# Kernel tuning notes

Hardware: AMD Instinct MI355X
Metric: run time of the kernel (lower is better)

## Reference

```python
import jax, jax.numpy as jnp
import numpy as np

E = 8192   # line-graph nodes (edges of g)
N = 4096   # graph nodes
FIN = 64   # in_feats
FOUT = 64  # out_feats
H = FOUT // 2
BN_EPS = 1e-5


def _linear_params(k, fan_in):
    kw, kb = jax.random.split(k)
    s = 1.0 / np.sqrt(fan_in)
    w = jax.random.uniform(kw, (H, fan_in), jnp.float32, -s, s)
    b = jax.random.uniform(kb, (H,), jnp.float32, -s, s)
    return w, b


def setup_inputs() -> dict:
    key = jax.random.key(0)
    ks = jax.random.split(key, 12)
    inp = {}
    inp["y"] = jax.random.normal(ks[0], (E, FIN), jnp.float32)
    inp["deg_g"] = jax.random.uniform(ks[1], (N,), jnp.float32)  # unused in forward
    inp["g_a1"] = jnp.zeros((N, N), jnp.float32)                  # unused in forward
    # adjacency-like 0/1 matrices, sparse pattern stored dense (as th.mm expects)
    inp["lg_a1"] = (jax.random.uniform(ks[2], (E, E)) < (8.0 / E)).astype(jnp.float32)
    inp["pm"] = (jax.random.uniform(ks[3], (N, E)) < (2.0 / N)).astype(jnp.float32)
    inp["pd"] = (jax.random.uniform(ks[4], (N, E)) < (2.0 / N)).astype(jnp.float32)
    inp["theta_y_w"], inp["theta_y_b"] = _linear_params(ks[5], FIN)
    inp["theta_y_r_w"], inp["theta_y_r_b"] = _linear_params(ks[6], FIN)
    inp["gamma_a_w"], inp["gamma_a_b"] = _linear_params(ks[7], FIN)
    inp["gamma_x_w"], inp["gamma_x_b"] = _linear_params(ks[8], FOUT)
    inp["gamma_a_r_w"], inp["gamma_a_r_b"] = _linear_params(ks[9], FIN)
    inp["gamma_x_r_w"], inp["gamma_x_r_b"] = _linear_params(ks[10], FOUT)
    inp["bn_x_w"] = jnp.ones((FOUT,), jnp.float32)
    inp["bn_x_b"] = jnp.zeros((FOUT,), jnp.float32)
    inp["bn_y_w"] = jnp.ones((FOUT,), jnp.float32)
    inp["bn_y_b"] = jnp.zeros((FOUT,), jnp.float32)
    return inp


def _bn(x, w, b):
    # BatchNorm2d on [B, C, 1, 1] in training mode == per-channel batch norm
    # with biased variance over the row (batch) dimension.
    m = x.mean(0)
    v = jnp.mean((x - m) ** 2, axis=0)
    return (x - m) * jax.lax.rsqrt(v + BN_EPS) * w + b


def reference(y, deg_g, g_a1, lg_a1, pm, pd,
              theta_y_w, theta_y_b, theta_y_r_w, theta_y_r_b,
              gamma_a_w, gamma_a_b, gamma_x_w, gamma_x_b,
              gamma_a_r_w, gamma_a_r_b, gamma_x_r_w, gamma_x_r_b,
              bn_x_w, bn_x_b, bn_y_w, bn_y_b):
    pd_y = pd @ y                                        # [N, FIN]
    x_r = pd_y @ theta_y_r_w.T + theta_y_r_b             # [N, H]
    x = pd_y @ theta_y_w.T + theta_y_b                   # [N, H]
    x = jnp.concatenate([x, jax.nn.relu(x_r)], axis=1)   # [N, FOUT]
    x = _bn(x, bn_x_w, bn_x_b)
    pm_x = pm.T @ x                                      # [E, FOUT]
    lg_y = lg_a1 @ y                                     # [E, FIN] (computed once; torch computes it twice, same math)
    y_r = (lg_y @ gamma_a_r_w.T + gamma_a_r_b) + (pm_x @ gamma_x_r_w.T + gamma_x_r_b)
    y_n = (lg_y @ gamma_a_w.T + gamma_a_b) + (pm_x @ gamma_x_w.T + gamma_x_b)
    y_out = jnp.concatenate([y_n, jax.nn.relu(y_r)], axis=1)  # [E, FOUT]
    return _bn(y_out, bn_y_w, bn_y_b)
```

## Files before the change

### kernel.cpp

```cpp
#include <hip/hip_runtime.h>

typedef unsigned int uint_t;
typedef unsigned short ushort_t;
typedef unsigned long long ull_t;
typedef uint_t nvec4 __attribute__((ext_vector_type(4)));

#define SLOTS 48

__device__ __forceinline__ float bcast(float v, int k) {
    union { float f; int i; } x; x.f = v;
    int r = __builtin_amdgcn_readlane(x.i, k);
    union { int i; float f; } y2; y2.i = r;
    return y2.f;
}

__global__ __launch_bounds__(256) void stream_gather_kernel(
    const float* __restrict__ lg, const float* __restrict__ pd,
    const float* __restrict__ pm, const float* __restrict__ y,
    float* __restrict__ lg_y, float* __restrict__ pd_y,
    ushort_t* __restrict__ pm_keys, uint_t* __restrict__ pm_counts)
{
    __shared__ ushort_t sIdx[4][SLOTS];
    const int lane = threadIdx.x & 63;
    const int wv = threadIdx.x >> 6;
    const int wid = blockIdx.x * 4 + wv;
    const float* A;
    int row;
    if (wid < 8192)       { row = wid;         A = lg; }
    else if (wid < 12288) { row = wid - 8192;  A = pd; }
    else                  { row = wid - 12288; A = pm; }

    const nvec4* ap = (const nvec4*)(A + (size_t)row * 8192);
    ushort_t* slice = sIdx[wv];
    const ull_t lt = (1ull << lane) - 1ull;

    nvec4 buf[16];
    #pragma unroll
    for (int i = 0; i < 16; ++i)
        buf[i] = __builtin_nontemporal_load(ap + i * 64 + lane);

    uint_t cnt = 0;
    #pragma unroll
    for (int pp = 0; pp < 32; pp += 16) {
        #pragma unroll
        for (int i = 0; i < 16; ++i) {
            nvec4 c = buf[i];
            if (pp == 0)
                buf[i] = __builtin_nontemporal_load(ap + (16 + i) * 64 + lane);
            uint_t a0 = c.x, a1 = c.y, a2 = c.z, a3 = c.w;
            ull_t m = __ballot((a0 | a1 | a2 | a3) != 0u);
            if (m) {
                ull_t m0 = __ballot(a0 != 0u);
                ull_t m1 = __ballot(a1 != 0u);
                ull_t m2 = __ballot(a2 != 0u);
                ull_t m3 = __ballot(a3 != 0u);
                uint_t c0 = (uint_t)__popcll(m0), c1 = (uint_t)__popcll(m1);
                uint_t c2 = (uint_t)__popcll(m2);
                uint_t o0 = cnt + (uint_t)__popcll(m0 & lt);
                uint_t o1 = cnt + c0 + (uint_t)__popcll(m1 & lt);
                uint_t o2 = cnt + c0 + c1 + (uint_t)__popcll(m2 & lt);
                uint_t o3 = cnt + c0 + c1 + c2 + (uint_t)__popcll(m3 & lt);
                int j = (pp + i) * 256 + lane * 4;
                if (a0 && o0 < SLOTS) slice[o0] = (ushort_t)(j + 0);
                if (a1 && o1 < SLOTS) slice[o1] = (ushort_t)(j + 1);
                if (a2 && o2 < SLOTS) slice[o2] = (ushort_t)(j + 2);
                if (a3 && o3 < SLOTS) slice[o3] = (ushort_t)(j + 3);
                cnt += (uint_t)(__popcll(m0) + __popcll(m1) +
                                __popcll(m2) + __popcll(m3));
            }
        }
    }
    if (cnt > SLOTS) cnt = SLOTS;

    if (wid >= 12288) {
        if (lane == 0) pm_counts[row] = cnt;
        if (lane < (int)cnt) pm_keys[(size_t)row * SLOTS + lane] = slice[lane];
        return;
    }
    float a0 = 0.f, a1 = 0.f, a2 = 0.f, a3 = 0.f;
    uint_t i = 0;
    for (; i + 4 <= cnt; i += 4) {
        int j0 = slice[i + 0], j1 = slice[i + 1];
        int j2 = slice[i + 2], j3 = slice[i + 3];
        a0 += y[(size_t)j0 * 64 + lane];
        a1 += y[(size_t)j1 * 64 + lane];
        a2 += y[(size_t)j2 * 64 + lane];
        a3 += y[(size_t)j3 * 64 + lane];
    }
    for (; i < cnt; ++i) a0 += y[(size_t)slice[i] * 64 + lane];
    float acc = (a0 + a1) + (a2 + a3);
    if (wid < 8192) lg_y[(size_t)row * 64 + lane] = acc;
    else            pd_y[(size_t)row * 64 + lane] = acc;
}

__global__ __launch_bounds__(256) void xscat_kernel(
    const float* __restrict__ pd_y,
    const ushort_t* __restrict__ pm_keys, const uint_t* __restrict__ pm_counts,
    const float* __restrict__ wt, const float* __restrict__ bt,
    const float* __restrict__ wr, const float* __restrict__ br,
    float* __restrict__ pm_x, float* __restrict__ deg,
    float* __restrict__ stats_x)
{
    __shared__ float red[2][4][64];
    const int wave = threadIdx.x >> 6, lane = threadIdx.x & 63;
    const int gwave = blockIdx.x * 4 + wave;

    float wreg[64];
    {
        const float* wsrc = (lane < 32) ? (wt + lane * 64)
                                        : (wr + (lane - 32) * 64);
        const float4* wp = (const float4*)wsrc;
        #pragma unroll
        for (int q = 0; q < 16; ++q) {
            float4 t = wp[q];
            wreg[q * 4 + 0] = t.x; wreg[q * 4 + 1] = t.y;
            wreg[q * 4 + 2] = t.z; wreg[q * 4 + 3] = t.w;
        }
    }
    float biasx = (lane < 32) ? bt[lane] : br[lane - 32];
    float xr[4];
    float s1 = 0.f, s2 = 0.f;
    const int xrow0 = gwave * 4;
    #pragma unroll
    for (int r = 0; r < 4; ++r) {
        float xv = pd_y[(size_t)(xrow0 + r) * 64 + lane];
        float acc = biasx;
        #pragma unroll
        for (int k = 0; k < 64; ++k) acc = fmaf(bcast(xv, k), wreg[k], acc);
        if (lane >= 32) acc = fmaxf(acc, 0.f);
        xr[r] = acc;
        s1 += acc; s2 += acc * acc;
    }
    red[0][wave][lane] = s1; red[1][wave][lane] = s2;
    __syncthreads();
    if (wave == 0) {
        float a = 0.f, b = 0.f;
        #pragma unroll
        for (int w = 0; w < 4; ++w) { a += red[0][w][lane]; b += red[1][w][lane]; }
        atomicAdd(&stats_x[lane], a);
        atomicAdd(&stats_x[64 + lane], b);
    }

    #pragma unroll
    for (int r = 0; r < 4; ++r) {
        int row = xrow0 + r;
        uint_t cnt = pm_counts[row];
        const ushort_t* slice = pm_keys + (size_t)row * SLOTS;
        for (uint_t i = 0; i < cnt; ++i) {
            int e = slice[i];
            atomicAdd(&pm_x[(size_t)e * 64 + lane], xr[r]);
            if (lane == 0) atomicAdd(&deg[e], 1.0f);
        }
    }
}

__global__ __launch_bounds__(256) void ylin_kernel(
    const float* __restrict__ lg_y, const float* __restrict__ pm_x,
    const float* __restrict__ deg, const float* __restrict__ stats_x,
    const float* __restrict__ bnxw, const float* __restrict__ bnxb,
    const float* __restrict__ wa, const float* __restrict__ ba,
    const float* __restrict__ wx, const float* __restrict__ bx,
    const float* __restrict__ war, const float* __restrict__ bar,
    const float* __restrict__ wxr, const float* __restrict__ bxr,
    float* __restrict__ yraw, float* __restrict__ stats_y)
{
    __shared__ float red[2][4][64];
    const int wave = threadIdx.x >> 6, lane = threadIdx.x & 63;
    const float* s1p = (lane < 32) ? (wa + lane * 64) : (war + (lane - 32) * 64);
    const float* s2p = (lane < 32) ? (wx + lane * 64) : (wxr + (lane - 32) * 64);
    float w1[64], w2[64];
    {
        const float4* p1 = (const float4*)s1p;
        const float4* p2 = (const float4*)s2p;
        #pragma unroll
        for (int q = 0; q < 16; ++q) {
            float4 t1 = p1[q], t2 = p2[q];
            w1[q * 4 + 0] = t1.x; w1[q * 4 + 1] = t1.y;
            w1[q * 4 + 2] = t1.z; w1[q * 4 + 3] = t1.w;
            w2[q * 4 + 0] = t2.x; w2[q * 4 + 1] = t2.y;
            w2[q * 4 + 2] = t2.z; w2[q * 4 + 3] = t2.w;
        }
    }
    float scx, shx;
    {
        float s = stats_x[lane];
        float q = stats_x[64 + lane];
        float mean = s * (1.f / 4096.f);
        float var  = fmaxf(q * (1.f / 4096.f) - mean * mean, 0.f);
        float rstd = rsqrtf(var + 1e-5f);
        scx = rstd * bnxw[lane];
        shx = bnxb[lane] - mean * scx;
    }
    float bias = (lane < 32) ? (ba[lane] + bx[lane])
                             : (bar[lane - 32] + bxr[lane - 32]);
    float s1 = 0.f, s2 = 0.f;
    const int row0 = (blockIdx.x * 4 + wave) * 8;
    for (int r = 0; r < 8; ++r) {
        int row = row0 + r;
        float lv = lg_y[(size_t)row * 64 + lane];
        float dg = deg[row];
        float pv = fmaf(pm_x[(size_t)row * 64 + lane], scx, shx * dg);
        float acc = bias;
        #pragma unroll
        for (int k = 0; k < 64; ++k) {
            acc = fmaf(bcast(lv, k), w1[k], acc);
            acc = fmaf(bcast(pv, k), w2[k], acc);
        }
        if (lane >= 32) acc = fmaxf(acc, 0.f);
        yraw[(size_t)row * 64 + lane] = acc;
        s1 += acc; s2 += acc * acc;
    }
    red[0][wave][lane] = s1; red[1][wave][lane] = s2;
    __syncthreads();
    if (wave == 0) {
        float a = 0.f, b = 0.f;
        #pragma unroll
        for (int w = 0; w < 4; ++w) { a += red[0][w][lane]; b += red[1][w][lane]; }
        atomicAdd(&stats_y[lane], a);
        atomicAdd(&stats_y[64 + lane], b);
    }
}

__global__ __launch_bounds__(256) void bny_kernel(
    float* __restrict__ yraw, const float* __restrict__ stats_y,
    const float* __restrict__ bnyw, const float* __restrict__ bnyb)
{
    int idx = blockIdx.x * 256 + threadIdx.x;
    int c = idx & 63;
    float mean = stats_y[c] * (1.f / 8192.f);
    float var  = fmaxf(stats_y[64 + c] * (1.f / 8192.f) - mean * mean, 0.f);
    float rstd = rsqrtf(var + 1e-5f);
    yraw[idx] = (yraw[idx] - mean) * rstd * bnyw[c] + bnyb[c];
}

extern "C" void kernel_launch(void* const* d_in, const int* in_sizes, int n_in,
                              void* d_out, int out_size, void* d_ws, size_t ws_size,
                              hipStream_t stream)
{
    const float* y     = (const float*)d_in[0];
    const float* lg_a1 = (const float*)d_in[3];
    const float* pm    = (const float*)d_in[4];
    const float* pd    = (const float*)d_in[5];
    const float* th_w  = (const float*)d_in[6];
    const float* th_b  = (const float*)d_in[7];
    const float* thr_w = (const float*)d_in[8];
    const float* thr_b = (const float*)d_in[9];
    const float* ga_w  = (const float*)d_in[10];
    const float* ga_b  = (const float*)d_in[11];
    const float* gx_w  = (const float*)d_in[12];
    const float* gx_b  = (const float*)d_in[13];
    const float* gar_w = (const float*)d_in[14];
    const float* gar_b = (const float*)d_in[15];
    const float* gxr_w = (const float*)d_in[16];
    const float* gxr_b = (const float*)d_in[17];
    const float* bnx_w = (const float*)d_in[18];
    const float* bnx_b = (const float*)d_in[19];
    const float* bny_w = (const float*)d_in[20];
    const float* bny_b = (const float*)d_in[21];

    char* ws = (char*)d_ws;
    float* stats_x = (float*)ws;
    float* stats_y = (float*)(ws + 1024);
    float* deg     = (float*)(ws + 2048);
    float* pm_x    = (float*)(ws + 2048 + 32768);
    const size_t zero_bytes = 2048 + 32768 + (size_t)8192 * 64 * 4;
    float* pd_y  = (float*)(ws + zero_bytes);
    float* lg_y  = pd_y + (size_t)4096 * 64;
    ushort_t* pm_keys = (ushort_t*)(lg_y + (size_t)8192 * 64);
    uint_t* pm_counts = (uint_t*)(pm_keys + (size_t)4096 * SLOTS);
    float* yraw  = (float*)d_out;

    (void)hipMemsetAsync(d_ws, 0, zero_bytes, stream);

    stream_gather_kernel<<<4096, 256, 0, stream>>>(lg_a1, pd, pm, y,
                                                   lg_y, pd_y,
                                                   pm_keys, pm_counts);
    xscat_kernel<<<256, 256, 0, stream>>>(pd_y, pm_keys, pm_counts,
                                          th_w, th_b, thr_w, thr_b,
                                          pm_x, deg, stats_x);
    ylin_kernel<<<256, 256, 0, stream>>>(lg_y, pm_x, deg, stats_x,
                                         bnx_w, bnx_b,
                                         ga_w, ga_b, gx_w, gx_b,
                                         gar_w, gar_b, gxr_w, gxr_b,
                                         yraw, stats_y);
    bny_kernel<<<2048, 256, 0, stream>>>(yraw, stats_y, bny_w, bny_b);
}
```

Before: 578.4 us.

## Fuse dense-matrix streaming gather with x linear and pm scatter into one kernel

Merges the streaming gather kernel and the x-scatter kernel into one launch. Waves 0-4095 each handle one graph node: they compact its pd row, gather y, apply the theta linear layer, compact its pm row and scatter into pm_x directly. The remaining waves handle two lg_a1 rows each. This removes one kernel launch and the pd_y and pm_keys round trips through global memory. In exchange it gives waves unequal work (node waves stream two rows plus the matmul and atomics) and holds 64 weight registers live in the streaming kernel, which may lower occupancy.

```diff
diff --git a/kernel.cpp b/kernel.cpp
--- a/kernel.cpp
+++ b/kernel.cpp
@@ -14,26 +14,9 @@
     return y2.f;
 }
 
-__global__ __launch_bounds__(256) void stream_gather_kernel(
-    const float* __restrict__ lg, const float* __restrict__ pd,
-    const float* __restrict__ pm, const float* __restrict__ y,
-    float* __restrict__ lg_y, float* __restrict__ pd_y,
-    ushort_t* __restrict__ pm_keys, uint_t* __restrict__ pm_counts)
-{
-    __shared__ ushort_t sIdx[4][SLOTS];
-    const int lane = threadIdx.x & 63;
-    const int wv = threadIdx.x >> 6;
-    const int wid = blockIdx.x * 4 + wv;
-    const float* A;
-    int row;
-    if (wid < 8192)       { row = wid;         A = lg; }
-    else if (wid < 12288) { row = wid - 8192;  A = pd; }
-    else                  { row = wid - 12288; A = pm; }
-
-    const nvec4* ap = (const nvec4*)(A + (size_t)row * 8192);
-    ushort_t* slice = sIdx[wv];
-    const ull_t lt = (1ull << lane) - 1ull;
-
+__device__ __forceinline__ uint_t stream_compact(const nvec4* ap, ushort_t* slice,
+                                                 int lane, ull_t lt)
+{
     nvec4 buf[16];
     #pragma unroll
     for (int i = 0; i < 16; ++i)
@@ -70,13 +53,12 @@
             }
         }
     }
-    if (cnt > SLOTS) cnt = SLOTS;
-
-    if (wid >= 12288) {
-        if (lane == 0) pm_counts[row] = cnt;
-        if (lane < (int)cnt) pm_keys[(size_t)row * SLOTS + lane] = slice[lane];
-        return;
-    }
+    return cnt;
+}
+
+__device__ __forceinline__ float gather_y(const ushort_t* slice, uint_t cnt,
+                                          const float* y, int lane)
+{
     float a0 = 0.f, a1 = 0.f, a2 = 0.f, a3 = 0.f;
     uint_t i = 0;
     for (; i + 4 <= cnt; i += 4) {
@@ -88,68 +70,78 @@
         a3 += y[(size_t)j3 * 64 + lane];
     }
     for (; i < cnt; ++i) a0 += y[(size_t)slice[i] * 64 + lane];
-    float acc = (a0 + a1) + (a2 + a3);
-    if (wid < 8192) lg_y[(size_t)row * 64 + lane] = acc;
-    else            pd_y[(size_t)row * 64 + lane] = acc;
-}
-
-__global__ __launch_bounds__(256) void xscat_kernel(
-    const float* __restrict__ pd_y,
-    const ushort_t* __restrict__ pm_keys, const uint_t* __restrict__ pm_counts,
+    return (a0 + a1) + (a2 + a3);
+}
+
+__global__ __launch_bounds__(256) void stream_fused_kernel(
+    const float* __restrict__ lg, const float* __restrict__ pd,
+    const float* __restrict__ pm, const float* __restrict__ y,
     const float* __restrict__ wt, const float* __restrict__ bt,
     const float* __restrict__ wr, const float* __restrict__ br,
-    float* __restrict__ pm_x, float* __restrict__ deg,
-    float* __restrict__ stats_x)
-{
+    float* __restrict__ lg_y, float* __restrict__ pm_x,
+    float* __restrict__ deg, float* __restrict__ stats_x)
+{
+    __shared__ ushort_t sIdx[4][SLOTS];
     __shared__ float red[2][4][64];
-    const int wave = threadIdx.x >> 6, lane = threadIdx.x & 63;
-    const int gwave = blockIdx.x * 4 + wave;
-
-    float wreg[64];
-    {
-        const float* wsrc = (lane < 32) ? (wt + lane * 64)
-                                        : (wr + (lane - 32) * 64);
-        const float4* wp = (const float4*)wsrc;
-        #pragma unroll
-        for (int q = 0; q < 16; ++q) {
-            float4 t = wp[q];
-            wreg[q * 4 + 0] = t.x; wreg[q * 4 + 1] = t.y;
-            wreg[q * 4 + 2] = t.z; wreg[q * 4 + 3] = t.w;
-        }
-    }
-    float biasx = (lane < 32) ? bt[lane] : br[lane - 32];
-    float xr[4];
-    float s1 = 0.f, s2 = 0.f;
-    const int xrow0 = gwave * 4;
-    #pragma unroll
-    for (int r = 0; r < 4; ++r) {
-        float xv = pd_y[(size_t)(xrow0 + r) * 64 + lane];
-        float acc = biasx;
+    const int lane = threadIdx.x & 63;
+    const int wv = threadIdx.x >> 6;
+    const int wid = blockIdx.x * 4 + wv;
+    ushort_t* slice = sIdx[wv];
+    const ull_t lt = (1ull << lane) - 1ull;
+
+    if (wid < 4096) {
+        const int n = wid;
+        uint_t cnt = stream_compact((const nvec4*)(pd + (size_t)n * 8192),
+                                    slice, lane, lt);
+        if (cnt > SLOTS) cnt = SLOTS;
+        float xv = gather_y(slice, cnt, y, lane);
+
+        float wreg[64];
+        {
+            const float* wsrc = (lane < 32) ? (wt + lane * 64)
+                                            : (wr + (lane - 32) * 64);
+            const float4* wp = (const float4*)wsrc;
+            #pragma unroll
+            for (int q = 0; q < 16; ++q) {
+                float4 t = wp[q];
+                wreg[q * 4 + 0] = t.x; wreg[q * 4 + 1] = t.y;
+                wreg[q * 4 + 2] = t.z; wreg[q * 4 + 3] = t.w;
+            }
+        }
+        float acc = (lane < 32) ? bt[lane] : br[lane - 32];
         #pragma unroll
         for (int k = 0; k < 64; ++k) acc = fmaf(bcast(xv, k), wreg[k], acc);
         if (lane >= 32) acc = fmaxf(acc, 0.f);
-        xr[r] = acc;
-        s1 += acc; s2 += acc * acc;
-    }
-    red[0][wave][lane] = s1; red[1][wave][lane] = s2;
-    __syncthreads();
-    if (wave == 0) {
-        float a = 0.f, b = 0.f;
-        #pragma unroll
-        for (int w = 0; w < 4; ++w) { a += red[0][w][lane]; b += red[1][w][lane]; }
-        atomicAdd(&stats_x[lane], a);
-        atomicAdd(&stats_x[64 + lane], b);
-    }
-
-    #pragma unroll
-    for (int r = 0; r < 4; ++r) {
-        int row = xrow0 + r;
-        uint_t cnt = pm_counts[row];
-        const ushort_t* slice = pm_keys + (size_t)row * SLOTS;
+
+        red[0][wv][lane] = acc;
+        red[1][wv][lane] = acc * acc;
+
+        cnt = stream_compact((const nvec4*)(pm + (size_t)n * 8192),
+                             slice, lane, lt);
+        if (cnt > SLOTS) cnt = SLOTS;
         for (uint_t i = 0; i < cnt; ++i) {
             int e = slice[i];
-            atomicAdd(&pm_x[(size_t)e * 64 + lane], xr[r]);
+            atomicAdd(&pm_x[(size_t)e * 64 + lane], acc);
             if (lane == 0) atomicAdd(&deg[e], 1.0f);
+        }
+
+        __syncthreads();
+        if (wv == 0) {
+            float a = 0.f, b = 0.f;
+            #pragma unroll
+            for (int w = 0; w < 4; ++w) { a += red[0][w][lane]; b += red[1][w][lane]; }
+            atomicAdd(&stats_x[lane], a);
+            atomicAdd(&stats_x[64 + lane], b);
+        }
+    } else {
+        const int r0 = (wid - 4096) * 2;
+        #pragma unroll
+        for (int rr = 0; rr < 2; ++rr) {
+            int row = r0 + rr;
+            uint_t cnt = stream_compact((const nvec4*)(lg + (size_t)row * 8192),
+                                        slice, lane, lt);
+            if (cnt > SLOTS) cnt = SLOTS;
+            lg_y[(size_t)row * 64 + lane] = gather_y(slice, cnt, y, lane);
         }
     }
 }
@@ -264,20 +256,14 @@
     float* deg     = (float*)(ws + 2048);
     float* pm_x    = (float*)(ws + 2048 + 32768);
     const size_t zero_bytes = 2048 + 32768 + (size_t)8192 * 64 * 4;
-    float* pd_y  = (float*)(ws + zero_bytes);
-    float* lg_y  = pd_y + (size_t)4096 * 64;
-    ushort_t* pm_keys = (ushort_t*)(lg_y + (size_t)8192 * 64);
-    uint_t* pm_counts = (uint_t*)(pm_keys + (size_t)4096 * SLOTS);
+    float* lg_y  = (float*)(ws + zero_bytes);
     float* yraw  = (float*)d_out;
 
     (void)hipMemsetAsync(d_ws, 0, zero_bytes, stream);
 
-    stream_gather_kernel<<<4096, 256, 0, stream>>>(lg_a1, pd, pm, y,
-                                                   lg_y, pd_y,
-                                                   pm_keys, pm_counts);
-    xscat_kernel<<<256, 256, 0, stream>>>(pd_y, pm_keys, pm_counts,
-                                          th_w, th_b, thr_w, thr_b,
-                                          pm_x, deg, stats_x);
+    stream_fused_kernel<<<2048, 256, 0, stream>>>(lg_a1, pd, pm, y,
+                                                  th_w, th_b, thr_w, thr_b,
+                                                  lg_y, pm_x, deg, stats_x);
     ylin_kernel<<<256, 256, 0, stream>>>(lg_y, pm_x, deg, stats_x,
                                          bnx_w, bnx_b,
                                          ga_w, ga_b, gx_w, gx_b,
```

Result: no change. 568.1 us (-1.8%).
